# Kernel tuning notes

Measured on AMD Instinct MI355X. Metric: run time of the kernel, lower is better.

The kernel has to match this reference:

```python
import jax, jax.numpy as jnp
import numpy as np

N_NODES = 50000
N_EDGES = 1_600_000
IN_DIM = 512
HIDDEN = 512
OUT_DIM = 128
K = 10
ALPHA = 0.1


def setup_inputs() -> dict:
    key = jax.random.key(0)
    ks = jax.random.split(key, 7)
    x = jax.random.normal(ks[0], (N_NODES, IN_DIM), dtype=jnp.float32)
    edge_index = jax.random.randint(ks[1], (2, N_EDGES), 0, N_NODES, dtype=jnp.int64)
    s_in = 1.0 / np.sqrt(IN_DIM)
    s_h = 1.0 / np.sqrt(HIDDEN)
    lin_in_w = jax.random.uniform(ks[2], (HIDDEN, IN_DIM), jnp.float32, -s_in, s_in)
    lin_in_b = jax.random.uniform(ks[3], (HIDDEN,), jnp.float32, -s_in, s_in)
    lin_out_w = jax.random.uniform(ks[4], (OUT_DIM, HIDDEN), jnp.float32, -s_h, s_h)
    lin_out_b = jax.random.uniform(ks[5], (OUT_DIM,), jnp.float32, -s_h, s_h)
    # GPR init: alpha*(1-alpha)^k, normalized
    w = np.array([ALPHA * (1 - ALPHA) ** k for k in range(K + 1)], dtype=np.float32)
    gpr_weights = jnp.asarray(w / w.sum())
    return {
        "x": x, "edge_index": edge_index,
        "lin_in_w": lin_in_w, "lin_in_b": lin_in_b,
        "lin_out_w": lin_out_w, "lin_out_b": lin_out_b,
        "gpr_weights": gpr_weights,
    }


def reference(x, edge_index, lin_in_w, lin_in_b, lin_out_w, lin_out_b, gpr_weights):
    n = x.shape[0]
    loops = jnp.arange(n, dtype=edge_index.dtype)
    row = jnp.concatenate([edge_index[0], loops])  # [E+n]
    col = jnp.concatenate([edge_index[1], loops])
    # degree over rows (edge_index_sl[0]), clamped to >=1
    deg = jax.ops.segment_sum(jnp.ones_like(row, dtype=x.dtype), row, num_segments=n)
    dis = jnp.clip(deg, 1.0) ** -0.5  # deg^-0.5, [n]

    h = jax.nn.relu(x @ lin_in_w.T + lin_in_b)  # [n, hidden] (dropout = identity in eval)
    w = jax.nn.softmax(gpr_weights)  # [K+1]

    def step(carry, wk):
        h_prop, acc = carry
        hs = h_prop * dis[:, None]
        h_prop = jax.ops.segment_sum(hs[col], row, num_segments=n) * dis[:, None]
        return (h_prop, acc + wk * h_prop), None

    (_, h_final), _ = jax.lax.scan(step, (h, w[0] * h), w[1:])
    return h_final @ lin_out_w.T + lin_out_b
```

## Files before the change

### kernel.cpp

```cpp
#include <hip/hip_runtime.h>


#define SLOTS 96
#define NB2   98
#define BCAP  18432
#define CHUNK 4096

typedef __attribute__((ext_vector_type(8))) short short8;
typedef __attribute__((ext_vector_type(4))) float f32x4;

__device__ inline ushort f2bf(float f) {
    uint x = __float_as_uint(f);
    return (ushort)((x + 0x7fffu + ((x >> 16) & 1u)) >> 16);
}
__device__ inline float bflo(uint u) { return __uint_as_float(u << 16); }
__device__ inline float bfhi(uint u) { return __uint_as_float(u & 0xffff0000u); }

__device__ __forceinline__ void glds16(const ushort* g, ushort* l) {
    __builtin_amdgcn_global_load_lds(
        (const __attribute__((address_space(1))) void*)g,
        (__attribute__((address_space(3))) void*)l, 16, 0, 0);
}

__global__ void init_kernel(int* __restrict__ gcur, int ngc,
                            ushort* __restrict__ yAll, size_t ystride, int zrow,
                            uint* __restrict__ cfill, int cfcnt, uint cfval) {
    const int gid = blockIdx.x * blockDim.x + threadIdx.x;
    const int stride = gridDim.x * blockDim.x;
    for (int i = gid; i < cfcnt; i += stride) cfill[i] = cfval;
    for (int i = gid; i < ngc; i += stride) gcur[i] = 0;
    for (int i = gid; i < 11 * 128; i += stride) {
        int k = i >> 7, d = i & 127;
        yAll[(size_t)k * ystride + (size_t)zrow * 128 + d] = 0;
    }
}

__global__ __launch_bounds__(512) void partition_kernel(
    const int* __restrict__ row, const int* __restrict__ col,
    int* __restrict__ gcur, uint* __restrict__ bbuf, int E) {
    __shared__ int cnt[128];
    __shared__ int base[128];
    __shared__ int gbase[128];
    __shared__ uint sbuf[CHUNK];
    const int tid = threadIdx.x;
    const int e0 = blockIdx.x * CHUNK;
    if (tid < 128) cnt[tid] = 0;
    __syncthreads();
    int myb[8]; int myp[8]; uint mye[8];
#pragma unroll
    for (int j = 0; j < 8; ++j) {
        int i = e0 + tid + j * 512;
        myb[j] = -1;
        if (i < E) {
            int r = row[i];
            int c = col[i];
            myb[j] = r >> 9;
            mye[j] = ((uint)(r & 511) << 16) | (uint)c;
            myp[j] = atomicAdd(&cnt[myb[j]], 1);
        }
    }
    __syncthreads();
    if (tid < 128) base[tid] = cnt[tid];
    __syncthreads();
    for (int off = 1; off < 128; off <<= 1) {
        int v = 0;
        if (tid < 128 && tid >= off) v = base[tid - off];
        __syncthreads();
        if (tid < 128) base[tid] += v;
        __syncthreads();
    }
    if (tid < 128) base[tid] -= cnt[tid];
    __syncthreads();
    if (tid < NB2 && cnt[tid] > 0) gbase[tid] = atomicAdd(&gcur[tid], cnt[tid]);
    __syncthreads();
#pragma unroll
    for (int j = 0; j < 8; ++j)
        if (myb[j] >= 0) sbuf[base[myb[j]] + myp[j]] = mye[j];
    __syncthreads();
    const int wv = tid >> 6, lane = tid & 63;
    for (int b = wv; b < NB2; b += 8) {
        const int len = cnt[b], src = base[b], dst = gbase[b];
        for (int i = lane; i < len; i += 64) {
            int d = dst + i;
            if (d < BCAP) bbuf[(size_t)b * BCAP + d] = sbuf[src + i];
        }
    }
}

__global__ __launch_bounds__(1024) void expand2_kernel(
    const int* __restrict__ gcur, const uint* __restrict__ bbuf,
    ushort* __restrict__ col_s, int* __restrict__ deg,
    float* __restrict__ dis, float* __restrict__ dis2, float* __restrict__ rdis,
    int n) {
    __shared__ int cur[128];
    const int b = blockIdx.x >> 2;
    const int q = blockIdx.x & 3;
    const int tid = threadIdx.x;
    if (tid < 128) cur[tid] = 0;
    __syncthreads();
    int cb = gcur[b];
    if (cb > BCAP) cb = BCAP;
    const size_t bb = (size_t)b * BCAP;
    const int rlo = q * 128, rhi = rlo + 128;
    for (int i = tid; i < cb; i += 1024) {
        uint e = bbuf[bb + i];
        int rl = (int)(e >> 16);
        if (rl >= rlo && rl < rhi) {
            int p = atomicAdd(&cur[rl - rlo], 1);
            if (p < SLOTS)
                col_s[((size_t)(b * 512 + rl)) * SLOTS + p] = (ushort)(e & 0xffffu);
        }
    }
    __syncthreads();
    if (tid < 128) {
        int r = b * 512 + rlo + tid;
        if (r < n) {
            int d = cur[tid];
            deg[r] = d;
            float fd = (float)(d + 1);
            float di = rsqrtf(fd);
            dis[r] = di;
            dis2[r] = di * di;
            rdis[r] = sqrtf(fd);
        }
    }
}

__global__ void cvt_all_kernel(const float* __restrict__ x,
                               const float* __restrict__ win,
                               const float* __restrict__ wout,
                               ushort* __restrict__ x_bf,
                               ushort* __restrict__ win_bf,
                               ushort* __restrict__ wout_bf,
                               int nx_src8, int nx8, int nw18, int nw28) {
    const int gid = blockIdx.x * blockDim.x + threadIdx.x;
    const int stride = gridDim.x * blockDim.x;
    const int tot = nx8 + nw18 + nw28;
    for (int i = gid; i < tot; i += stride) {
        const float* src;
        ushort* dst;
        int idx;
        if (i < nx8) {
            if (i >= nx_src8) {
                short8 z = (short8)0;
                *reinterpret_cast<short8*>(x_bf + (size_t)i * 8) = z;
                continue;
            }
            src = x; dst = x_bf; idx = i;
        } else if (i < nx8 + nw18) {
            src = win; dst = win_bf; idx = i - nx8;
        } else {
            src = wout; dst = wout_bf; idx = i - nx8 - nw18;
        }
        const float4* s = reinterpret_cast<const float4*>(src + (size_t)idx * 8);
        float4 a = s[0], b = s[1];
        short8 o;
        o[0] = (short)f2bf(a.x); o[1] = (short)f2bf(a.y);
        o[2] = (short)f2bf(a.z); o[3] = (short)f2bf(a.w);
        o[4] = (short)f2bf(b.x); o[5] = (short)f2bf(b.y);
        o[6] = (short)f2bf(b.z); o[7] = (short)f2bf(b.w);
        *reinterpret_cast<short8*>(dst + (size_t)idx * 8) = o;
    }
}

__global__ __launch_bounds__(512) void gemm1_kernel(
    const ushort* __restrict__ A, const ushort* __restrict__ B,
    const float* __restrict__ bias, ushort* __restrict__ outH, int M) {
    __shared__ __align__(16) ushort As[128 * 32];
    __shared__ __align__(16) ushort Bs[256 * 32];
    const int tid = threadIdx.x;
    const int lane = tid & 63;
    const int w = tid >> 6;
    const int wm = (w >> 2) * 64, wn = (w & 3) * 64;
    const int bm = blockIdx.y * 128, bn = blockIdx.x * 256;
    const int lrow = lane & 15, lk8 = (lane >> 4) * 8;

    f32x4 acc[4][4];
#pragma unroll
    for (int i = 0; i < 4; ++i)
#pragma unroll
        for (int j = 0; j < 4; ++j) acc[i][j] = (f32x4)(0.f);

    const int arow = 16 * w + (lane >> 2);
    const int acol = (lane & 3) * 8;
    const ushort* gA = A + (size_t)(bm + arow) * 512 + acol;
    const ushort* gB0 = B + (size_t)(bn + 32 * w + (lane >> 2)) * 512 + acol;
    const ushort* gB1 = gB0 + (size_t)16 * 512;
    ushort* lA = As + w * 512;
    ushort* lB0 = Bs + w * 1024;
    ushort* lB1 = Bs + w * 1024 + 512;

    for (int k0 = 0; k0 < 512; k0 += 32) {
        glds16(gA + k0, lA);
        glds16(gB0 + k0, lB0);
        glds16(gB1 + k0, lB1);
        __syncthreads();
        short8 af[4], bfr[4];
#pragma unroll
        for (int mf = 0; mf < 4; ++mf)
            af[mf] = *reinterpret_cast<const short8*>(As + (wm + mf * 16 + lrow) * 32 + lk8);
#pragma unroll
        for (int nf = 0; nf < 4; ++nf)
            bfr[nf] = *reinterpret_cast<const short8*>(Bs + (wn + nf * 16 + lrow) * 32 + lk8);
#pragma unroll
        for (int mf = 0; mf < 4; ++mf)
#pragma unroll
            for (int nf = 0; nf < 4; ++nf)
                acc[mf][nf] = __builtin_amdgcn_mfma_f32_16x16x32_bf16(af[mf], bfr[nf], acc[mf][nf], 0, 0, 0);
        __syncthreads();
    }

#pragma unroll
    for (int mf = 0; mf < 4; ++mf) {
#pragma unroll
        for (int nf = 0; nf < 4; ++nf) {
            const int col = bn + wn + nf * 16 + lrow;
#pragma unroll
            for (int r = 0; r < 4; ++r) {
                const int row = bm + wm + mf * 16 + (lane >> 4) * 4 + r;
                if (row < M) {
                    float v = fmaxf(acc[mf][nf][r] + bias[col], 0.f);
                    outH[(size_t)row * 512 + col] = f2bf(v);
                }
            }
        }
    }
}

__global__ __launch_bounds__(256) void gemm2_kernel(
    const ushort* __restrict__ A, const ushort* __restrict__ B,
    const float* __restrict__ dis, ushort* __restrict__ outY, int M) {
    __shared__ __align__(16) ushort As[128 * 32];
    __shared__ __align__(16) ushort Bs[128 * 32];
    const int tid = threadIdx.x;
    const int lane = tid & 63;
    const int w = tid >> 6;
    const int wm = (w >> 1) * 64, wn = (w & 1) * 64;
    const int bm = blockIdx.x * 128;
    const int lrow = lane & 15, lk8 = (lane >> 4) * 8;

    f32x4 acc[4][4];
#pragma unroll
    for (int i = 0; i < 4; ++i)
#pragma unroll
        for (int j = 0; j < 4; ++j) acc[i][j] = (f32x4)(0.f);

    const int sub = 32 * w + (lane >> 2);
    const int acol = (lane & 3) * 8;
    const ushort* gA0 = A + (size_t)(bm + sub) * 512 + acol;
    const ushort* gA1 = gA0 + (size_t)16 * 512;
    const ushort* gB0 = B + (size_t)sub * 512 + acol;
    const ushort* gB1 = gB0 + (size_t)16 * 512;
    ushort* lA0 = As + w * 1024;
    ushort* lA1 = As + w * 1024 + 512;
    ushort* lB0 = Bs + w * 1024;
    ushort* lB1 = Bs + w * 1024 + 512;

    for (int k0 = 0; k0 < 512; k0 += 32) {
        glds16(gA0 + k0, lA0);
        glds16(gA1 + k0, lA1);
        glds16(gB0 + k0, lB0);
        glds16(gB1 + k0, lB1);
        __syncthreads();
        short8 af[4], bfr[4];
#pragma unroll
        for (int mf = 0; mf < 4; ++mf)
            af[mf] = *reinterpret_cast<const short8*>(As + (wm + mf * 16 + lrow) * 32 + lk8);
#pragma unroll
        for (int nf = 0; nf < 4; ++nf)
            bfr[nf] = *reinterpret_cast<const short8*>(Bs + (wn + nf * 16 + lrow) * 32 + lk8);
#pragma unroll
        for (int mf = 0; mf < 4; ++mf)
#pragma unroll
            for (int nf = 0; nf < 4; ++nf)
                acc[mf][nf] = __builtin_amdgcn_mfma_f32_16x16x32_bf16(af[mf], bfr[nf], acc[mf][nf], 0, 0, 0);
        __syncthreads();
    }

#pragma unroll
    for (int mf = 0; mf < 4; ++mf) {
#pragma unroll
        for (int nf = 0; nf < 4; ++nf) {
            const int col = wn + nf * 16 + lrow;
#pragma unroll
            for (int r = 0; r < 4; ++r) {
                const int row = bm + wm + mf * 16 + (lane >> 4) * 4 + r;
                if (row < M)
                    outY[(size_t)row * 128 + col] = f2bf(dis[row] * acc[mf][nf][r]);
            }
        }
    }
}

__global__ __launch_bounds__(256) void spmm128_kernel(
    const int* __restrict__ deg, const ushort* __restrict__ col_s,
    const float* __restrict__ dis2,
    const ushort* __restrict__ y_old, ushort* __restrict__ y_new, int n) {
    int wid = (blockIdx.x * 256 + threadIdx.x) >> 6;
    if (wid >= n) return;
    wid = __builtin_amdgcn_readfirstlane(wid);
    const int lane = threadIdx.x & 63;
    int cnt = deg[wid];
    if (cnt > SLOTS) cnt = SLOTS;
    const int cnt8 = (cnt + 7) & ~7;
    const ushort* __restrict__ cp = col_s + (size_t)wid * SLOTS;
    const uint* __restrict__ Y = reinterpret_cast<const uint*>(y_old);
    float s0a = 0.f, s1a = 0.f, s0b = 0.f, s1b = 0.f;
    int t = 0;
    for (; t + 16 <= cnt8; t += 16) {
        int c[16];
        uint v[16];
#pragma unroll
        for (int j = 0; j < 16; ++j) c[j] = (int)cp[t + j];
#pragma unroll
        for (int j = 0; j < 16; ++j) v[j] = Y[(size_t)c[j] * 64 + lane];
#pragma unroll
        for (int j = 0; j < 16; ++j) {
            if (j & 1) { s0b += bflo(v[j]); s1b += bfhi(v[j]); }
            else       { s0a += bflo(v[j]); s1a += bfhi(v[j]); }
        }
    }
    if (t < cnt8) {
        int c[8];
        uint v[8];
#pragma unroll
        for (int j = 0; j < 8; ++j) c[j] = (int)cp[t + j];
#pragma unroll
        for (int j = 0; j < 8; ++j) v[j] = Y[(size_t)c[j] * 64 + lane];
#pragma unroll
        for (int j = 0; j < 8; ++j) {
            if (j & 1) { s0b += bflo(v[j]); s1b += bfhi(v[j]); }
            else       { s0a += bflo(v[j]); s1a += bfhi(v[j]); }
        }
    }
    const uint u = Y[(size_t)wid * 64 + lane];
    const float d2 = dis2[wid];
    const float y0 = d2 * (bflo(u) + (s0a + s0b));
    const float y1 = d2 * (bfhi(u) + (s1a + s1b));
    const uint pv = (uint)f2bf(y0) | ((uint)f2bf(y1) << 16);
    __builtin_nontemporal_store(pv, &reinterpret_cast<uint*>(y_new)[(size_t)wid * 64 + lane]);
}

__global__ __launch_bounds__(256) void finsum_kernel(
    const ushort* __restrict__ yAll, size_t ystride_dw,
    const float* __restrict__ gpr, const float* __restrict__ rdis,
    const float* __restrict__ bout, float* __restrict__ outp, int n) {
    __shared__ float w[11];
    if (threadIdx.x == 0) {
        float m = gpr[0];
        for (int i = 1; i < 11; ++i) m = fmaxf(m, gpr[i]);
        float e[11], s = 0.f;
        for (int i = 0; i < 11; ++i) { e[i] = expf(gpr[i] - m); s += e[i]; }
        float inv = 1.f / s;
        for (int i = 0; i < 11; ++i) w[i] = e[i] * inv;
    }
    __syncthreads();
    const int gid = blockIdx.x * 256 + threadIdx.x;
    if (gid >= n * 64) return;
    const int row = gid >> 6;
    const int lane = gid & 63;
    const uint* __restrict__ Y = reinterpret_cast<const uint*>(yAll);
    float s0 = 0.f, s1 = 0.f;
#pragma unroll
    for (int k = 0; k < 11; ++k) {
        const uint v = Y[k * ystride_dw + (size_t)row * 64 + lane];
        const float wk = w[k];
        s0 = fmaf(wk, bflo(v), s0);
        s1 = fmaf(wk, bfhi(v), s1);
    }
    const float r = rdis[row];
    float2 o;
    o.x = fmaf(s0, r, bout[lane * 2 + 0]);
    o.y = fmaf(s1, r, bout[lane * 2 + 1]);
    *reinterpret_cast<float2*>(outp + (size_t)row * 128 + lane * 2) = o;
}

extern "C" void kernel_launch(void* const* d_in, const int* in_sizes, int n_in,
                              void* d_out, int out_size, void* d_ws, size_t ws_size,
                              hipStream_t stream) {
    const float* x    = (const float*)d_in[0];
    const int*   ei   = (const int*)d_in[1];
    const float* win  = (const float*)d_in[2];
    const float* bin  = (const float*)d_in[3];
    const float* wout = (const float*)d_in[4];
    const float* bout = (const float*)d_in[5];
    const float* gpr  = (const float*)d_in[6];
    float* out = (float*)d_out;

    const int n = in_sizes[0] / 512;
    const int E = in_sizes[1] / 2;
    const int Mpad = ((n + 127) / 128) * 128;
    const int NPAD = NB2 * 512;

    char* ws = (char*)d_ws;
    size_t off = 0;
    auto take = [&](size_t bytes) -> char* {
        char* p = ws + off;
        off += (bytes + 511) & ~(size_t)511;
        return p;
    };
    int*    deg     = (int*)take((size_t)n * sizeof(int));
    float*  dis     = (float*)take((size_t)n * sizeof(float));
    float*  dis2    = (float*)take((size_t)n * sizeof(float));
    float*  rdis    = (float*)take((size_t)n * sizeof(float));
    int*    gcur    = (int*)take(128 * sizeof(int));
    uint*   bbuf    = (uint*)take((size_t)NB2 * BCAP * sizeof(uint));
    ushort* col_s   = (ushort*)take((size_t)NPAD * SLOTS * sizeof(ushort));
    ushort* x_bf    = (ushort*)take((size_t)Mpad * 512 * sizeof(ushort));
    ushort* win_bf  = (ushort*)take((size_t)512 * 512 * sizeof(ushort));
    ushort* wout_bf = (ushort*)take((size_t)128 * 512 * sizeof(ushort));
    ushort* h_bf    = (ushort*)take((size_t)Mpad * 512 * sizeof(ushort));
    const size_t ystride = (size_t)Mpad * 128;
    ushort* yAll    = (ushort*)take(11 * ystride * sizeof(ushort));

    const int* rowp = ei;
    const int* colp = ei + E;

    init_kernel<<<2048, 256, 0, stream>>>(gcur, 128, yAll, ystride, n,
                                          (uint*)col_s, NPAD * SLOTS / 2,
                                          ((uint)n << 16) | (uint)n);
    partition_kernel<<<(E + CHUNK - 1) / CHUNK, 512, 0, stream>>>(rowp, colp, gcur, bbuf, E);
    expand2_kernel<<<NB2 * 4, 1024, 0, stream>>>(gcur, bbuf, col_s, deg, dis, dis2, rdis, n);

    cvt_all_kernel<<<2048, 256, 0, stream>>>(x, win, wout, x_bf, win_bf, wout_bf,
                                             n * 64, Mpad * 64, 512 * 64, 128 * 64);

    dim3 g1(2, Mpad / 128);
    gemm1_kernel<<<g1, 512, 0, stream>>>(x_bf, win_bf, bin, h_bf, n);

    gemm2_kernel<<<Mpad / 128, 256, 0, stream>>>(h_bf, wout_bf, dis, yAll, n);

    const int spmm_blocks = (n + 3) / 4;
    for (int k = 1; k <= 10; ++k) {
        spmm128_kernel<<<spmm_blocks, 256, 0, stream>>>(
            deg, col_s, dis2, yAll + (size_t)(k - 1) * ystride, yAll + (size_t)k * ystride, n);
    }

    finsum_kernel<<<(n * 64 + 255) / 256, 256, 0, stream>>>(
        yAll, ystride / 2, gpr, rdis, bout, out, n);
}
```

Before: 637.7 us.

## Fuse final SpMM hop with weighted sum and drop full col_s prefill

The tenth propagation step is merged into the final weighted-sum kernel. y10 is computed in registers and never written to memory, and one launch is removed. The full-buffer fill of the padded column-index array is replaced by padding only each row's tail up to a multiple of 8 inside expand2. The softmax of the GPR weights moves into init_kernel, and the SpMM output store changes from nontemporal to a normal store. The tail-only padding relies on nothing reading slots beyond the rounded count.

```diff
diff --git a/kernel.cpp b/kernel.cpp
--- a/kernel.cpp
+++ b/kernel.cpp
@@ -24,10 +24,17 @@
 
 __global__ void init_kernel(int* __restrict__ gcur, int ngc,
                             ushort* __restrict__ yAll, size_t ystride, int zrow,
-                            uint* __restrict__ cfill, int cfcnt, uint cfval) {
+                            const float* __restrict__ gpr, float* __restrict__ w11) {
     const int gid = blockIdx.x * blockDim.x + threadIdx.x;
     const int stride = gridDim.x * blockDim.x;
-    for (int i = gid; i < cfcnt; i += stride) cfill[i] = cfval;
+    if (gid == 0) {
+        float m = gpr[0];
+        for (int i = 1; i < 11; ++i) m = fmaxf(m, gpr[i]);
+        float e[11], s = 0.f;
+        for (int i = 0; i < 11; ++i) { e[i] = expf(gpr[i] - m); s += e[i]; }
+        float inv = 1.f / s;
+        for (int i = 0; i < 11; ++i) w11[i] = e[i] * inv;
+    }
     for (int i = gid; i < ngc; i += stride) gcur[i] = 0;
     for (int i = gid; i < 11 * 128; i += stride) {
         int k = i >> 7, d = i & 127;
@@ -122,6 +129,11 @@
             dis[r] = di;
             dis2[r] = di * di;
             rdis[r] = sqrtf(fd);
+            int pstart = d < SLOTS ? d : SLOTS;
+            int pend = (pstart + 7) & ~7;
+            if (pend > SLOTS) pend = SLOTS;
+            ushort* cp = col_s + (size_t)r * SLOTS;
+            for (int p = pstart; p < pend; ++p) cp[p] = (ushort)n;
         }
     }
 }
@@ -337,42 +349,72 @@
     const float d2 = dis2[wid];
     const float y0 = d2 * (bflo(u) + (s0a + s0b));
     const float y1 = d2 * (bfhi(u) + (s1a + s1b));
-    const uint pv = (uint)f2bf(y0) | ((uint)f2bf(y1) << 16);
-    __builtin_nontemporal_store(pv, &reinterpret_cast<uint*>(y_new)[(size_t)wid * 64 + lane]);
-}
-
-__global__ __launch_bounds__(256) void finsum_kernel(
+    reinterpret_cast<uint*>(y_new)[(size_t)wid * 64 + lane] =
+        (uint)f2bf(y0) | ((uint)f2bf(y1) << 16);
+}
+
+__global__ __launch_bounds__(256) void spmm_last_kernel(
+    const int* __restrict__ deg, const ushort* __restrict__ col_s,
+    const float* __restrict__ dis2, const float* __restrict__ rdis,
     const ushort* __restrict__ yAll, size_t ystride_dw,
-    const float* __restrict__ gpr, const float* __restrict__ rdis,
-    const float* __restrict__ bout, float* __restrict__ outp, int n) {
-    __shared__ float w[11];
-    if (threadIdx.x == 0) {
-        float m = gpr[0];
-        for (int i = 1; i < 11; ++i) m = fmaxf(m, gpr[i]);
-        float e[11], s = 0.f;
-        for (int i = 0; i < 11; ++i) { e[i] = expf(gpr[i] - m); s += e[i]; }
-        float inv = 1.f / s;
-        for (int i = 0; i < 11; ++i) w[i] = e[i] * inv;
-    }
-    __syncthreads();
-    const int gid = blockIdx.x * 256 + threadIdx.x;
-    if (gid >= n * 64) return;
-    const int row = gid >> 6;
-    const int lane = gid & 63;
+    const float* __restrict__ w11, const float* __restrict__ bout,
+    float* __restrict__ outp, int n) {
+    int wid = (blockIdx.x * 256 + threadIdx.x) >> 6;
+    if (wid >= n) return;
+    wid = __builtin_amdgcn_readfirstlane(wid);
+    const int lane = threadIdx.x & 63;
+    const uint* __restrict__ Y9 = reinterpret_cast<const uint*>(yAll) + 9 * ystride_dw;
+    int cnt = deg[wid];
+    if (cnt > SLOTS) cnt = SLOTS;
+    const int cnt8 = (cnt + 7) & ~7;
+    const ushort* __restrict__ cp = col_s + (size_t)wid * SLOTS;
+    float s0a = 0.f, s1a = 0.f, s0b = 0.f, s1b = 0.f;
+    int t = 0;
+    for (; t + 16 <= cnt8; t += 16) {
+        int c[16];
+        uint v[16];
+#pragma unroll
+        for (int j = 0; j < 16; ++j) c[j] = (int)cp[t + j];
+#pragma unroll
+        for (int j = 0; j < 16; ++j) v[j] = Y9[(size_t)c[j] * 64 + lane];
+#pragma unroll
+        for (int j = 0; j < 16; ++j) {
+            if (j & 1) { s0b += bflo(v[j]); s1b += bfhi(v[j]); }
+            else       { s0a += bflo(v[j]); s1a += bfhi(v[j]); }
+        }
+    }
+    if (t < cnt8) {
+        int c[8];
+        uint v[8];
+#pragma unroll
+        for (int j = 0; j < 8; ++j) c[j] = (int)cp[t + j];
+#pragma unroll
+        for (int j = 0; j < 8; ++j) v[j] = Y9[(size_t)c[j] * 64 + lane];
+#pragma unroll
+        for (int j = 0; j < 8; ++j) {
+            if (j & 1) { s0b += bflo(v[j]); s1b += bfhi(v[j]); }
+            else       { s0a += bflo(v[j]); s1a += bfhi(v[j]); }
+        }
+    }
+    const uint u9 = Y9[(size_t)wid * 64 + lane];
+    const float d2 = dis2[wid];
+    const float y10_0 = d2 * (bflo(u9) + (s0a + s0b));
+    const float y10_1 = d2 * (bfhi(u9) + (s1a + s1b));
+    const float w10 = w11[10];
+    float s0 = w10 * y10_0, s1 = w10 * y10_1;
     const uint* __restrict__ Y = reinterpret_cast<const uint*>(yAll);
-    float s0 = 0.f, s1 = 0.f;
-#pragma unroll
-    for (int k = 0; k < 11; ++k) {
-        const uint v = Y[k * ystride_dw + (size_t)row * 64 + lane];
-        const float wk = w[k];
+#pragma unroll
+    for (int k = 0; k < 10; ++k) {
+        const uint v = Y[k * ystride_dw + (size_t)wid * 64 + lane];
+        const float wk = w11[k];
         s0 = fmaf(wk, bflo(v), s0);
         s1 = fmaf(wk, bfhi(v), s1);
     }
-    const float r = rdis[row];
+    const float r = rdis[wid];
     float2 o;
     o.x = fmaf(s0, r, bout[lane * 2 + 0]);
     o.y = fmaf(s1, r, bout[lane * 2 + 1]);
-    *reinterpret_cast<float2*>(outp + (size_t)row * 128 + lane * 2) = o;
+    *reinterpret_cast<float2*>(outp + (size_t)wid * 128 + lane * 2) = o;
 }
 
 extern "C" void kernel_launch(void* const* d_in, const int* in_sizes, int n_in,
@@ -403,6 +445,7 @@
     float*  dis     = (float*)take((size_t)n * sizeof(float));
     float*  dis2    = (float*)take((size_t)n * sizeof(float));
     float*  rdis    = (float*)take((size_t)n * sizeof(float));
+    float*  w11     = (float*)take(16 * sizeof(float));
     int*    gcur    = (int*)take(128 * sizeof(int));
     uint*   bbuf    = (uint*)take((size_t)NB2 * BCAP * sizeof(uint));
     ushort* col_s   = (ushort*)take((size_t)NPAD * SLOTS * sizeof(ushort));
@@ -416,9 +459,7 @@
     const int* rowp = ei;
     const int* colp = ei + E;
 
-    init_kernel<<<2048, 256, 0, stream>>>(gcur, 128, yAll, ystride, n,
-                                          (uint*)col_s, NPAD * SLOTS / 2,
-                                          ((uint)n << 16) | (uint)n);
+    init_kernel<<<64, 256, 0, stream>>>(gcur, 128, yAll, ystride, n, gpr, w11);
     partition_kernel<<<(E + CHUNK - 1) / CHUNK, 512, 0, stream>>>(rowp, colp, gcur, bbuf, E);
     expand2_kernel<<<NB2 * 4, 1024, 0, stream>>>(gcur, bbuf, col_s, deg, dis, dis2, rdis, n);
 
@@ -431,11 +472,11 @@
     gemm2_kernel<<<Mpad / 128, 256, 0, stream>>>(h_bf, wout_bf, dis, yAll, n);
 
     const int spmm_blocks = (n + 3) / 4;
-    for (int k = 1; k <= 10; ++k) {
+    for (int k = 1; k <= 9; ++k) {
         spmm128_kernel<<<spmm_blocks, 256, 0, stream>>>(
             deg, col_s, dis2, yAll + (size_t)(k - 1) * ystride, yAll + (size_t)k * ystride, n);
     }
 
-    finsum_kernel<<<(n * 64 + 255) / 256, 256, 0, stream>>>(
-        yAll, ystride / 2, gpr, rdis, bout, out, n);
-}
+    spmm_last_kernel<<<spmm_blocks, 256, 0, stream>>>(
+        deg, col_s, dis2, rdis, yAll, ystride / 2, w11, bout, out, n);
+}
```

Measured after the change: 631.6 us (median of 2 runs). About the same (-1.0%).
